# Kernel tuning notes

Measured on AMD Instinct MI355X. Metric: run time of the kernel, lower is better.

Reference implementation:

```python
import jax, jax.numpy as jnp
import numpy as np

D = 1024
H = 16
DEPTH = D // H


def setup_inputs() -> dict:
    key = jax.random.key(0)
    ks = jax.random.split(key, 9)
    s = 1.0 / np.sqrt(D)
    return {
        "x": jax.random.normal(ks[0], (2, 2048, D), dtype=jnp.float32),
        "Wq": jax.random.uniform(ks[1], (D, D), jnp.float32, -s, s),
        "bq": jax.random.uniform(ks[2], (D,), jnp.float32, -s, s),
        "Wk": jax.random.uniform(ks[3], (D, D), jnp.float32, -s, s),
        "bk": jax.random.uniform(ks[4], (D,), jnp.float32, -s, s),
        "Wv": jax.random.uniform(ks[5], (D, D), jnp.float32, -s, s),
        "bv": jax.random.uniform(ks[6], (D,), jnp.float32, -s, s),
        "Wo": jax.random.uniform(ks[7], (D, D), jnp.float32, -s, s),
        "bo": jax.random.uniform(ks[8], (D,), jnp.float32, -s, s),
    }


def _split_heads(t):
    b, s, _ = t.shape
    return t.reshape(b, s, H, DEPTH).transpose(0, 2, 1, 3)  # [B,H,S,depth]


def reference(x, Wq, bq, Wk, bk, Wv, bv, Wo, bo):
    q = _split_heads(x @ Wq.T + bq)
    k = _split_heads(x @ Wk.T + bk)
    v = _split_heads(x @ Wv.T + bv)
    scores = jnp.einsum("bhqd,bhkd->bhqk", q, k) / jnp.sqrt(jnp.float32(DEPTH))
    weights = jax.nn.softmax(scores, axis=-1)
    attn = jnp.einsum("bhqk,bhkd->bhqd", weights, v)
    b, _, s, _ = attn.shape
    attn = attn.transpose(0, 2, 1, 3).reshape(b, s, D)
    return attn @ Wo.T + bo
```

## Files before the change

### kernel.cpp

```cpp
#include <hip/hip_runtime.h>
#include <hip/hip_bf16.h>


typedef __bf16 bf16x8 __attribute__((ext_vector_type(8)));
typedef float f32x4 __attribute__((ext_vector_type(4)));
typedef unsigned short u16;
typedef unsigned short u16x4 __attribute__((ext_vector_type(4)));
typedef unsigned short u16x8 __attribute__((ext_vector_type(8)));
typedef unsigned int u32x2 __attribute__((ext_vector_type(2)));

__device__ __forceinline__ u16 f2bf(float f) {
  union { float f; unsigned u; } x; x.f = f;
  return (u16)((x.u + 0x7fffu + ((x.u >> 16) & 1u)) >> 16);
}

__device__ __forceinline__ void load_lds16(const void* g, void* l) {
  __builtin_amdgcn_global_load_lds((const __attribute__((address_space(1))) void*)g,
                                   (__attribute__((address_space(3))) void*)l,
                                   16, 0, 0);
}

__device__ __forceinline__ bf16x8 frag128(const u16* base, int row, int ch) {
  return *(const bf16x8*)((const char*)base + row * 128 + (((ch) ^ (row & 7)) << 4));
}

__device__ __forceinline__ float exp2_hw(float x) {
  float r;
  asm("v_exp_f32 %0, %1" : "=v"(r) : "v"(x));
  return r;
}

__device__ __forceinline__ unsigned cvt_pk_bf16(float lo, float hi) {
  unsigned r;
  asm("v_cvt_pk_bf16_f32 %0, %1, %2" : "=v"(r) : "v"(lo), "v"(hi));
  return r;
}

__device__ __forceinline__ bf16x8 mk8(unsigned a, unsigned b, unsigned c,
                                      unsigned d) {
  union { unsigned u[4]; bf16x8 v; } x;
  x.u[0] = a; x.u[1] = b; x.u[2] = c; x.u[3] = d;
  return x.v;
}

__global__ __launch_bounds__(256) void cvt_all(
    const float* __restrict__ x, const float* __restrict__ wq,
    const float* __restrict__ wk, const float* __restrict__ wv,
    const float* __restrict__ wo, u16* __restrict__ dst) {
  int i = blockIdx.x * 256 + threadIdx.x;
  const float* src;
  int loc;
  if (i < 1048576) {
    src = x; loc = i;
  } else {
    int j = i - 1048576;
    int seg = j >> 18;
    loc = j & 262143;
    src = (seg == 0) ? wq : (seg == 1) ? wk : (seg == 2) ? wv : wo;
  }
  f32x4 v = ((const f32x4*)src)[loc];
  u16x4 o;
#pragma unroll
  for (int j = 0; j < 4; ++j) o[j] = f2bf(v[j]);
  ((u16x4*)dst)[i] = o;
}

template <int BM, int MODE>
__global__ __launch_bounds__(256) void gemm_bf16(
    const u16* __restrict__ A, const u16* __restrict__ Bw,
    const float* __restrict__ bias0, const float* __restrict__ bias1,
    const float* __restrict__ bias2,
    u16* __restrict__ o_q, u16* __restrict__ o_k, u16* __restrict__ o_vt,
    float* __restrict__ o_f, int K) {
  constexpr int MBF = BM / 32;
  __shared__ u16 sA[BM * 64];
  __shared__ u16 sB[128 * 64];
  const int tid = threadIdx.x, l = tid & 63, w = tid >> 6;
  const int wr = w >> 1, wc = w & 1;
  const int lr = l & 15, lq = l >> 4;
  const int m0 = blockIdx.y * BM, n0 = blockIdx.x * 128;

  f32x4 acc[MBF][4];
#pragma unroll
  for (int mb = 0; mb < MBF; ++mb)
#pragma unroll
    for (int nb = 0; nb < 4; ++nb) acc[mb][nb] = f32x4{0.f, 0.f, 0.f, 0.f};

  const int nkt = K / 64;
  for (int kt = 0; kt < nkt; ++kt) {
#pragma unroll
    for (int i = 0; i < BM / 32; ++i) {
      int p = (i * 4 + w) * 1024 + l * 16;
      int row = p >> 7, ch = ((p >> 4) & 7) ^ (row & 7);
      load_lds16(A + (size_t)(m0 + row) * K + kt * 64 + ch * 8,
                 (char*)sA + (i * 4 + w) * 1024);
    }
#pragma unroll
    for (int i = 0; i < 4; ++i) {
      int p = (i * 4 + w) * 1024 + l * 16;
      int row = p >> 7, ch = ((p >> 4) & 7) ^ (row & 7);
      load_lds16(Bw + (size_t)(n0 + row) * K + kt * 64 + ch * 8,
                 (char*)sB + (i * 4 + w) * 1024);
    }
    __syncthreads();
#pragma unroll
    for (int ks = 0; ks < 2; ++ks) {
      bf16x8 af[MBF], bfr[4];
#pragma unroll
      for (int mb = 0; mb < MBF; ++mb)
        af[mb] = frag128(sA, wr * (BM / 2) + mb * 16 + lr, lq + 4 * ks);
#pragma unroll
      for (int nb = 0; nb < 4; ++nb)
        bfr[nb] = frag128(sB, wc * 64 + nb * 16 + lr, lq + 4 * ks);
#pragma unroll
      for (int mb = 0; mb < MBF; ++mb)
#pragma unroll
        for (int nb = 0; nb < 4; ++nb)
          acc[mb][nb] = __builtin_amdgcn_mfma_f32_16x16x32_bf16(
              af[mb], bfr[nb], acc[mb][nb], 0, 0, 0);
    }
    __syncthreads();
  }

#pragma unroll
  for (int nb = 0; nb < 4; ++nb) {
    const int n = n0 + wc * 64 + nb * 16 + lr;
    if constexpr (MODE == 0) {
      const int qkv = n >> 10, c = n & 1023;
      const float* bp = (qkv == 0) ? bias0 : ((qkv == 1) ? bias1 : bias2);
      const float bv = bp[c];
      const int h = c >> 6, d = c & 63;
      if (qkv == 2) {
#pragma unroll
        for (int mb = 0; mb < MBF; ++mb) {
          int mbase = m0 + wr * (BM / 2) + mb * 16 + lq * 4;
          int b = mbase >> 11, s0 = mbase & 2047;
          u16x4 pk;
#pragma unroll
          for (int r = 0; r < 4; ++r) pk[r] = f2bf(acc[mb][nb][r] + bv);
          *(u16x4*)(o_vt + ((size_t)((b * 16 + h) * 64 + d)) * 2048 + s0) = pk;
        }
      } else {
        u16* dp = (qkv == 0) ? o_q : o_k;
#pragma unroll
        for (int mb = 0; mb < MBF; ++mb)
#pragma unroll
          for (int r = 0; r < 4; ++r) {
            int m = m0 + wr * (BM / 2) + mb * 16 + lq * 4 + r;
            int b = m >> 11, s = m & 2047;
            float v = acc[mb][nb][r] + bv;
            if (qkv == 0) v *= 0.18033688011f;
            dp[((size_t)(b * 16 + h) * 2048 + s) * 64 + d] = f2bf(v);
          }
      }
    } else {
      const float bv = bias0[n];
#pragma unroll
      for (int mb = 0; mb < MBF; ++mb)
#pragma unroll
        for (int r = 0; r < 4; ++r) {
          int m = m0 + wr * (BM / 2) + mb * 16 + lq * 4 + r;
          o_f[(size_t)m * 1024 + n] = acc[mb][nb][r] + bv;
        }
    }
  }
}

__global__ __launch_bounds__(256, 2) void attn_fwd(
    const u16* __restrict__ q16, const u16* __restrict__ k16,
    const u16* __restrict__ vt16, u16* __restrict__ att16) {
  __shared__ u16 sK[2][128 * 64];
  __shared__ u16 sV[2][64 * 128];
  const int tid = threadIdx.x, l = tid & 63, w = tid >> 6;
  const int lr = l & 15, lq = l >> 4;
  const int lin = (blockIdx.y << 4) | blockIdx.x;
  const int wg = (lin & 7) * 64 + (lin >> 3);
  const int qt = wg & 15, bh = wg >> 4;
  const int b = bh >> 4, h = bh & 15;
  const char* kg = (const char*)(k16 + (size_t)bh * 2048 * 64);
  const char* vg = (const char*)(vt16 + (size_t)bh * 64 * 2048);

  bf16x8 aq[2][2];
#pragma unroll
  for (int mb = 0; mb < 2; ++mb)
#pragma unroll
    for (int ks = 0; ks < 2; ++ks) {
      int qrow = qt * 128 + w * 32 + mb * 16 + lr;
      aq[mb][ks] = *(const bf16x8*)(q16 + ((size_t)bh * 2048 + qrow) * 64 +
                                    ks * 32 + lq * 8);
    }

  const int krow0 = tid >> 3, kch = tid & 7;
  const int vrow0 = tid >> 4, vch = tid & 15;

  f32x4 kbuf[4], vbuf[4];
#pragma unroll
  for (int j = 0; j < 4; ++j)
    kbuf[j] = *(const f32x4*)(kg + j * 4096 + tid * 16);
#pragma unroll
  for (int j = 0; j < 4; ++j)
    vbuf[j] = *(const f32x4*)(vg + (size_t)(j * 16 + vrow0) * 4096 + vch * 16);
#pragma unroll
  for (int j = 0; j < 4; ++j) {
    int row = j * 32 + krow0;
    *(f32x4*)((char*)sK[0] + row * 128 + ((kch ^ (row & 7)) << 4)) = kbuf[j];
  }
#pragma unroll
  for (int j = 0; j < 4; ++j) {
    int row = j * 16 + vrow0;
    *(f32x4*)((char*)sV[0] + row * 256 + ((vch ^ (row & 7)) << 4)) = vbuf[j];
  }
#pragma unroll
  for (int j = 0; j < 4; ++j)
    kbuf[j] = *(const f32x4*)(kg + 16384 + j * 4096 + tid * 16);
#pragma unroll
  for (int j = 0; j < 4; ++j)
    vbuf[j] = *(const f32x4*)(vg + (size_t)(j * 16 + vrow0) * 4096 +
                              256 + vch * 16);
  __syncthreads();

  f32x4 o[2][4];
#pragma unroll
  for (int mb = 0; mb < 2; ++mb)
#pragma unroll
    for (int db = 0; db < 4; ++db) o[mb][db] = f32x4{0.f, 0.f, 0.f, 0.f};
  float l_run[2] = {0.f, 0.f};

  for (int kt = 0; kt < 16; ++kt) {
    const int cur = kt & 1;
    const u16* sKc = sK[cur];
    const u16* sVc = sV[cur];

    f32x4 s[2][8];
#pragma unroll
    for (int mb = 0; mb < 2; ++mb)
#pragma unroll
      for (int nb = 0; nb < 8; ++nb) s[mb][nb] = f32x4{0.f, 0.f, 0.f, 0.f};
    __builtin_amdgcn_s_setprio(1);
#pragma unroll
    for (int ks = 0; ks < 2; ++ks) {
#pragma unroll
      for (int g = 0; g < 2; ++g) {
        bf16x8 bk[4];
#pragma unroll
        for (int j = 0; j < 4; ++j)
          bk[j] = frag128(sKc, (g * 4 + j) * 16 + lr, lq + 4 * ks);
#pragma unroll
        for (int j = 0; j < 4; ++j)
#pragma unroll
          for (int mb = 0; mb < 2; ++mb)
            s[mb][g * 4 + j] = __builtin_amdgcn_mfma_f32_16x16x32_bf16(
                bk[j], aq[mb][ks], s[mb][g * 4 + j], 0, 0, 0);
      }
    }
    __builtin_amdgcn_s_setprio(0);

#pragma unroll
    for (int mb = 0; mb < 2; ++mb) {
      float rs = 0.f;
#pragma unroll
      for (int nb = 0; nb < 8; ++nb)
#pragma unroll
        for (int r = 0; r < 4; ++r) {
          float p_ = exp2_hw(s[mb][nb][r]);
          s[mb][nb][r] = p_;
          rs += p_;
        }
      l_run[mb] += rs;
    }

#pragma unroll
    for (int g = 0; g < 4; ++g) {
      bf16x8 ap[2];
#pragma unroll
      for (int mb = 0; mb < 2; ++mb)
        ap[mb] = mk8(cvt_pk_bf16(s[mb][2 * g][0], s[mb][2 * g][1]),
                     cvt_pk_bf16(s[mb][2 * g][2], s[mb][2 * g][3]),
                     cvt_pk_bf16(s[mb][2 * g + 1][0], s[mb][2 * g + 1][1]),
                     cvt_pk_bf16(s[mb][2 * g + 1][2], s[mb][2 * g + 1][3]));
      bf16x8 bv[4];
#pragma unroll
      for (int db = 0; db < 4; ++db) {
        int row = db * 16 + lr;
        const char* rb = (const char*)sVc + row * 256;
        int sw = row & 7;
        u32x2 lo = *(const u32x2*)(rb + ((((4 * g + (lq >> 1)) ^ sw) << 4) +
                                         8 * (lq & 1)));
        u32x2 hi = *(const u32x2*)(rb + ((((4 * g + 2 + (lq >> 1)) ^ sw) << 4) +
                                         8 * (lq & 1)));
        bv[db] = mk8(lo[0], lo[1], hi[0], hi[1]);
      }
      __builtin_amdgcn_s_setprio(1);
#pragma unroll
      for (int db = 0; db < 4; ++db)
#pragma unroll
        for (int mb = 0; mb < 2; ++mb)
          o[mb][db] = __builtin_amdgcn_mfma_f32_16x16x32_bf16(
              ap[mb], bv[db], o[mb][db], 0, 0, 0);
      __builtin_amdgcn_s_setprio(0);
    }

    if (kt < 15) {
      u16* sKn = sK[cur ^ 1];
      u16* sVn = sV[cur ^ 1];
#pragma unroll
      for (int j = 0; j < 4; ++j) {
        int row = j * 32 + krow0;
        *(f32x4*)((char*)sKn + row * 128 + ((kch ^ (row & 7)) << 4)) = kbuf[j];
      }
#pragma unroll
      for (int j = 0; j < 4; ++j) {
        int row = j * 16 + vrow0;
        *(f32x4*)((char*)sVn + row * 256 + ((vch ^ (row & 7)) << 4)) = vbuf[j];
      }
      if (kt < 14) {
#pragma unroll
        for (int j = 0; j < 4; ++j)
          kbuf[j] = *(const f32x4*)(kg + (size_t)(kt + 2) * 16384 +
                                    j * 4096 + tid * 16);
#pragma unroll
        for (int j = 0; j < 4; ++j)
          vbuf[j] = *(const f32x4*)(vg + (size_t)(j * 16 + vrow0) * 4096 +
                                    (kt + 2) * 256 + vch * 16);
      }
    }
    __syncthreads();
  }

#pragma unroll
  for (int mb = 0; mb < 2; ++mb) {
    float lv = l_run[mb];
    lv += __shfl_xor(lv, 16, 64);
    lv += __shfl_xor(lv, 32, 64);
    float inv[4];
#pragma unroll
    for (int r = 0; r < 4; ++r) inv[r] = 1.f / __shfl(lv, lq * 4 + r, 64);
#pragma unroll
    for (int db = 0; db < 4; ++db)
#pragma unroll
      for (int r = 0; r < 4; ++r) {
        float v = o[mb][db][r] * inv[r];
        int qg_ = qt * 128 + w * 32 + mb * 16 + lq * 4 + r;
        int col = h * 64 + db * 16 + lr;
        att16[((size_t)(b * 2048 + qg_)) * 1024 + col] = f2bf(v);
      }
  }
}

extern "C" void kernel_launch(void* const* d_in, const int* in_sizes, int n_in,
                              void* d_out, int out_size, void* d_ws, size_t ws_size,
                              hipStream_t stream) {
  const float* x  = (const float*)d_in[0];
  const float* Wq = (const float*)d_in[1];
  const float* bq = (const float*)d_in[2];
  const float* Wk = (const float*)d_in[3];
  const float* bk = (const float*)d_in[4];
  const float* Wv = (const float*)d_in[5];
  const float* bv = (const float*)d_in[6];
  const float* Wo = (const float*)d_in[7];
  const float* bo = (const float*)d_in[8];
  float* out = (float*)d_out;

  char* ws = (char*)d_ws;
  const size_t MB = 1024 * 1024;
  if (ws_size < 40 * MB) return;
  u16* x16  = (u16*)(ws);
  u16* w16  = (u16*)(ws + 8 * MB);
  u16* q16  = (u16*)(ws + 16 * MB);
  u16* k16  = (u16*)(ws + 24 * MB);
  u16* vt16 = (u16*)(ws + 32 * MB);
  u16* att16 = x16;

  cvt_all<<<8192, 256, 0, stream>>>(x, Wq, Wk, Wv, Wo, x16);

  gemm_bf16<128, 0><<<dim3(24, 32), 256, 0, stream>>>(
      x16, w16, bq, bk, bv, q16, k16, vt16, nullptr, 1024);

  attn_fwd<<<dim3(16, 32), 256, 0, stream>>>(q16, k16, vt16, att16);

  gemm_bf16<64, 1><<<dim3(8, 64), 256, 0, stream>>>(
      att16, w16 + 3145728, bo, nullptr, nullptr, nullptr, nullptr, nullptr,
      out, 1024);
}
```

Measured before the change: 113.7 us.

## Use direct global-to-LDS loads for attention K/V and swizzle GEMM block order

The attention kernel now fills the K and V tiles with global_load_lds instead of staging them through registers, using the same XOR-swizzled layout. The next tile is issued at the start of each iteration into the other buffer, so the prefetch depth drops from two tiles to one. This frees the register staging buffers and the explicit LDS store instructions. Separately, the GEMM remaps linear block IDs in groups of eight, intended to improve L2 or cache locality across workgroups.

```diff
diff --git a/kernel.cpp b/kernel.cpp
--- a/kernel.cpp
+++ b/kernel.cpp
@@ -73,12 +73,16 @@
     u16* __restrict__ o_q, u16* __restrict__ o_k, u16* __restrict__ o_vt,
     float* __restrict__ o_f, int K) {
   constexpr int MBF = BM / 32;
+  constexpr int NBX = (MODE == 0) ? 24 : 8;
+  constexpr int NBY = (MODE == 0) ? 32 : 64;
   __shared__ u16 sA[BM * 64];
   __shared__ u16 sB[128 * 64];
   const int tid = threadIdx.x, l = tid & 63, w = tid >> 6;
   const int wr = w >> 1, wc = w & 1;
   const int lr = l & 15, lq = l >> 4;
-  const int m0 = blockIdx.y * BM, n0 = blockIdx.x * 128;
+  const int lin = blockIdx.y * NBX + blockIdx.x;
+  const int wgs = (lin & 7) * (NBX * NBY / 8) + (lin >> 3);
+  const int m0 = (wgs / NBX) * BM, n0 = (wgs % NBX) * 128;
 
   f32x4 acc[MBF][4];
 #pragma unroll
@@ -190,33 +194,22 @@
                                     ks * 32 + lq * 8);
     }
 
-  const int krow0 = tid >> 3, kch = tid & 7;
-  const int vrow0 = tid >> 4, vch = tid & 15;
-
-  f32x4 kbuf[4], vbuf[4];
-#pragma unroll
-  for (int j = 0; j < 4; ++j)
-    kbuf[j] = *(const f32x4*)(kg + j * 4096 + tid * 16);
-#pragma unroll
-  for (int j = 0; j < 4; ++j)
-    vbuf[j] = *(const f32x4*)(vg + (size_t)(j * 16 + vrow0) * 4096 + vch * 16);
-#pragma unroll
-  for (int j = 0; j < 4; ++j) {
-    int row = j * 32 + krow0;
-    *(f32x4*)((char*)sK[0] + row * 128 + ((kch ^ (row & 7)) << 4)) = kbuf[j];
-  }
-#pragma unroll
-  for (int j = 0; j < 4; ++j) {
-    int row = j * 16 + vrow0;
-    *(f32x4*)((char*)sV[0] + row * 256 + ((vch ^ (row & 7)) << 4)) = vbuf[j];
-  }
-#pragma unroll
-  for (int j = 0; j < 4; ++j)
-    kbuf[j] = *(const f32x4*)(kg + 16384 + j * 4096 + tid * 16);
-#pragma unroll
-  for (int j = 0; j < 4; ++j)
-    vbuf[j] = *(const f32x4*)(vg + (size_t)(j * 16 + vrow0) * 4096 +
-                              256 + vch * 16);
+  int koff[4], voff[4];
+#pragma unroll
+  for (int i = 0; i < 4; ++i) {
+    int p = (i * 4 + w) * 1024 + l * 16;
+    int krow = p >> 7, kch = ((p >> 4) & 7) ^ (krow & 7);
+    koff[i] = krow * 128 + kch * 16;
+    int vrow = p >> 8, vch = ((p >> 4) & 15) ^ (vrow & 7);
+    voff[i] = vrow * 4096 + vch * 16;
+  }
+
+#pragma unroll
+  for (int i = 0; i < 4; ++i)
+    load_lds16(kg + koff[i], (char*)sK[0] + (i * 4 + w) * 1024);
+#pragma unroll
+  for (int i = 0; i < 4; ++i)
+    load_lds16(vg + voff[i], (char*)sV[0] + (i * 4 + w) * 1024);
   __syncthreads();
 
   f32x4 o[2][4];
@@ -230,6 +223,19 @@
     const int cur = kt & 1;
     const u16* sKc = sK[cur];
     const u16* sVc = sV[cur];
+
+    if (kt < 15) {
+      char* dK = (char*)sK[cur ^ 1];
+      char* dV = (char*)sV[cur ^ 1];
+#pragma unroll
+      for (int i = 0; i < 4; ++i)
+        load_lds16(kg + (size_t)(kt + 1) * 16384 + koff[i],
+                   dK + (i * 4 + w) * 1024);
+#pragma unroll
+      for (int i = 0; i < 4; ++i)
+        load_lds16(vg + (size_t)(kt + 1) * 256 + voff[i],
+                   dV + (i * 4 + w) * 1024);
+    }
 
     f32x4 s[2][8];
 #pragma unroll
@@ -300,30 +306,6 @@
       __builtin_amdgcn_s_setprio(0);
     }
 
-    if (kt < 15) {
-      u16* sKn = sK[cur ^ 1];
-      u16* sVn = sV[cur ^ 1];
-#pragma unroll
-      for (int j = 0; j < 4; ++j) {
-        int row = j * 32 + krow0;
-        *(f32x4*)((char*)sKn + row * 128 + ((kch ^ (row & 7)) << 4)) = kbuf[j];
-      }
-#pragma unroll
-      for (int j = 0; j < 4; ++j) {
-        int row = j * 16 + vrow0;
-        *(f32x4*)((char*)sVn + row * 256 + ((vch ^ (row & 7)) << 4)) = vbuf[j];
-      }
-      if (kt < 14) {
-#pragma unroll
-        for (int j = 0; j < 4; ++j)
-          kbuf[j] = *(const f32x4*)(kg + (size_t)(kt + 2) * 16384 +
-                                    j * 4096 + tid * 16);
-#pragma unroll
-        for (int j = 0; j < 4; ++j)
-          vbuf[j] = *(const f32x4*)(vg + (size_t)(j * 16 + vrow0) * 4096 +
-                                    (kt + 2) * 256 + vch * 16);
-      }
-    }
     __syncthreads();
   }
 
```

After: 111.3 us. 2.1% less time.
